# Kernel tuning notes

Measured on AMD Instinct MI355X. Metric: run time of the kernel, lower is better.

Reference implementation:

```python
import jax, jax.numpy as jnp
import numpy as np

N, E, B, F, H = 50000, 600000, 256, 128, 128
RATIO = 0.8
BN_EPS = 1e-5


def _topk_keep(score, batch, mask):
    # Per-graph top-ceil(RATIO*live) selection, expressed as a fixed-size keep mask.
    s = jnp.where(mask, score, -jnp.inf)
    order = jnp.lexsort((-s, batch))  # primary: batch id, secondary: score desc
    rank = jnp.zeros(N, dtype=jnp.int32).at[order].set(jnp.arange(N, dtype=jnp.int32))
    total = jax.ops.segment_sum(jnp.ones(N, dtype=jnp.int32), batch, B)
    starts = jnp.cumsum(total) - total
    r_in_g = (rank - starts[batch]).astype(jnp.float32)  # rank within own graph
    live = jax.ops.segment_sum(mask.astype(jnp.float32), batch, B)
    k = jnp.ceil(RATIO * live)
    return (r_in_g < k[batch]) & mask


def _forward(x, edge_index, batch, W1s, b1s, W2s, b2s, gammas, betas, pool_ws):
    src, dst = edge_index[0], edge_index[1]
    mask = jnp.ones(N, dtype=bool)      # live-node mask (TopK pooling shrinks graphs)
    e_mask = jnp.ones(E, dtype=bool)    # live-edge mask
    out = jnp.zeros((B, 2 * H), dtype=x.dtype)
    for i in range(4):
        # GINConv (eps=0): MLP(x + sum_{j->i} x_j)
        msg = jnp.where(e_mask[:, None], x[src], 0.0)
        agg = jax.ops.segment_sum(msg, dst, num_segments=N)
        h = x + agg
        h = jax.nn.relu(h @ W1s[i] + b1s[i]) @ W2s[i] + b2s[i]
        # BatchNorm (training mode) over live nodes only
        m = mask[:, None].astype(h.dtype)
        n = jnp.maximum(jnp.sum(m), 1.0)
        mean = jnp.sum(h * m, axis=0) / n
        var = jnp.sum(((h - mean) ** 2) * m, axis=0) / n
        h = (h - mean) * jax.lax.rsqrt(var + BN_EPS) * gammas[i] + betas[i]
        h = jax.nn.relu(h) * m
        # TopKPooling(ratio=0.8): score = x@w/||w||, keep top-k per graph, scale by tanh
        w = pool_ws[i]
        score = (h @ w) / jnp.linalg.norm(w)
        keep = _topk_keep(score, batch, mask)
        x = jnp.where(keep[:, None], h * jnp.tanh(score)[:, None], 0.0)
        mask = keep
        e_mask = e_mask & keep[src] & keep[dst]
        # global max pool + global mean pool over live nodes
        mx = jax.ops.segment_max(jnp.where(mask[:, None], x, -jnp.inf), batch, num_segments=B)
        mx = jnp.where(jnp.isfinite(mx), mx, 0.0)
        cnt = jax.ops.segment_sum(mask.astype(x.dtype), batch, num_segments=B)
        mn = jax.ops.segment_sum(x, batch, num_segments=B) / jnp.maximum(cnt, 1.0)[:, None]
        out = out + jnp.concatenate([mx, mn], axis=1)  # x1 + x2 + x3 + x4
    return out


def setup_inputs() -> dict:
    key = jax.random.key(0)
    k = jax.random.split(key, 8)
    s = 1.0 / np.sqrt(H)
    return {
        "x": jax.random.normal(k[0], (N, F), jnp.float32),
        "edge_index": jax.random.randint(k[1], (2, E), 0, N),
        "batch": jnp.sort(jax.random.randint(k[2], (N,), 0, B)),
        "W1s": jax.random.normal(k[3], (4, F, H), jnp.float32) * s,
        "b1s": jax.random.normal(k[4], (4, H), jnp.float32) * s,
        "W2s": jax.random.normal(k[5], (4, H, H), jnp.float32) * s,
        "b2s": jax.random.normal(k[6], (4, H), jnp.float32) * s,
        "gammas": jnp.ones((4, H), jnp.float32),
        "betas": jnp.zeros((4, H), jnp.float32),
        "pool_ws": jax.random.normal(k[7], (4, H), jnp.float32) * s,
    }


def reference(x, edge_index, batch, W1s, b1s, W2s, b2s, gammas, betas, pool_ws):
    return _forward(x, edge_index, batch, W1s, b1s, W2s, b2s, gammas, betas, pool_ws)
```

## Files before the change

### kernel.cpp

```cpp
#include <hip/hip_runtime.h>
#include <hip/hip_bf16.h>
#include <math.h>


#define HF 128
#define CHUNK_LG 14

typedef __attribute__((ext_vector_type(8))) short short8;
typedef __attribute__((ext_vector_type(4))) float floatx4;

__device__ __forceinline__ unsigned short cvt_bf16(float f) {
    unsigned u = __float_as_uint(f);
    u = u + 0x7fffu + ((u >> 16) & 1u);
    return (unsigned short)(u >> 16);
}
__device__ __forceinline__ float bf16f(unsigned short h) {
    return __uint_as_float(((unsigned)h) << 16);
}

__device__ __forceinline__ void split3(float f, short& p1, short& p2, short& p3) {
    unsigned u = __float_as_uint(f);
    unsigned r = u + 0x7fffu + ((u >> 16) & 1u);
    p1 = (short)(r >> 16);
    float r1 = f - __uint_as_float(r & 0xffff0000u);
    unsigned u1 = __float_as_uint(r1);
    p2 = (short)(u1 >> 16);
    float r2 = r1 - __uint_as_float(u1 & 0xffff0000u);
    p3 = (short)(__float_as_uint(r2) >> 16);
}


__global__ __launch_bounds__(256)
void k_hist(const int* __restrict__ dst, unsigned int* __restrict__ partial,
            unsigned char* __restrict__ eslot,
            float* __restrict__ stats4, float* __restrict__ out,
            int* __restrict__ lc,
            int N, int E, int nd4, int outsz, int X) {
    __shared__ unsigned int lh[12544];
    int bl = blockIdx.x, tid = threadIdx.x;
    for (int i = tid; i < nd4; i += 256) lh[i] = 0;
    __syncthreads();
    int e0 = bl << CHUNK_LG;
    int e1 = min(E, e0 + (1 << CHUNK_LG));
    for (int e = e0 + tid; e < e1; e += 256) {
        int d = dst[e];
        unsigned int old = atomicAdd(&lh[d >> 2], 1u << (8 * (d & 3)));
        eslot[e] = (unsigned char)((old >> (8 * (d & 3))) & 255u);
    }
    __syncthreads();
    for (int i = tid; i < nd4; i += 256) partial[(size_t)bl * nd4 + i] = lh[i];
    int gt = bl * 256 + tid, tot = X * 256;
    for (int i = gt; i < 4 * 256; i += tot) stats4[i] = 0.f;
    for (int i = gt; i < outsz; i += tot) out[i] = 0.f;
    if (gt < 5) lc[gt] = (gt == 0) ? N : 0;
}

__global__ __launch_bounds__(256)
void k_colsum(const unsigned int* __restrict__ partial, unsigned int* __restrict__ baseoff,
              int* __restrict__ deg, int* __restrict__ blocksum,
              int nd4, int X, int N) {
    __shared__ int red[256];
    int tid = threadIdx.x;
    int d4 = blockIdx.x * 256 + tid;
    unsigned int run = 0;
    if (d4 < nd4) {
        for (int bl = 0; bl < X; ++bl) {
            unsigned int c = partial[(size_t)bl * nd4 + d4];
            baseoff[(size_t)bl * nd4 + d4] = run;
            run += c;
        }
        int d = d4 * 4;
#pragma unroll
        for (int j = 0; j < 4; ++j)
            if (d + j < N) deg[d + j] = (int)((run >> (8 * j)) & 255u);
    }
    int tsum = (int)((run & 255u) + ((run >> 8) & 255u) + ((run >> 16) & 255u) + ((run >> 24) & 255u));
    red[tid] = tsum;
    __syncthreads();
    for (int off = 128; off; off >>= 1) {
        if (tid < off) red[tid] += red[tid + off];
        __syncthreads();
    }
    if (tid == 0) blocksum[blockIdx.x] = red[0];
}

__global__ void k_mid(const int* __restrict__ blocksum, int* __restrict__ blockoff,
                      int nblk, const int* __restrict__ batch,
                      int* __restrict__ gstart, int B, int n,
                      const float* __restrict__ pw, float* __restrict__ normv4) {
    int t = threadIdx.x;
    if (t <= B) {
        int lo = 0, hi = n;
        while (lo < hi) { int mid = (lo + hi) >> 1; if (batch[mid] < t) lo = mid + 1; else hi = mid; }
        gstart[t] = lo;
    }
    if (t >= 508) {
        int l = t - 508;
        float s = 0.f;
        for (int j = 0; j < HF; ++j) { float wv = pw[l * HF + j]; s += wv * wv; }
        normv4[l] = sqrtf(s);
    }
    if (t < 64) {
        int b0 = (t < nblk) ? blocksum[t] : 0;
        int v = b0;
#pragma unroll
        for (int off = 1; off < 64; off <<= 1) {
            int u = __shfl_up(v, off, 64);
            if (t >= off) v += u;
        }
        if (t < nblk) blockoff[t] = v - b0;
    }
}

__global__ __launch_bounds__(256)
void k_indptr(const int* __restrict__ deg, const int* __restrict__ blockoff,
              int* __restrict__ indptr, int nd4, int N) {
    __shared__ int ss[256];
    int tid = threadIdx.x;
    int d4 = blockIdx.x * 256 + tid;
    int dv[4] = {0, 0, 0, 0};
    int tsum = 0;
    if (d4 < nd4) {
        int d = d4 * 4;
#pragma unroll
        for (int j = 0; j < 4; ++j)
            if (d + j < N) { dv[j] = deg[d + j]; tsum += dv[j]; }
    }
    ss[tid] = tsum;
    __syncthreads();
    for (int off = 1; off < 256; off <<= 1) {
        int v = (tid >= off) ? ss[tid - off] : 0;
        __syncthreads();
        ss[tid] += v;
        __syncthreads();
    }
    if (d4 < nd4) {
        int b = blockoff[blockIdx.x] + ss[tid] - tsum;
        int d = d4 * 4;
#pragma unroll
        for (int j = 0; j < 4; ++j)
            if (d + j < N) { indptr[d + j] = b; b += dv[j]; }
        if (d4 == (N - 1) >> 2) indptr[N] = b;
    }
}

__global__ __launch_bounds__(256)
void k_place(const int* __restrict__ src, const int* __restrict__ dst,
             const unsigned char* __restrict__ eslot, const unsigned int* __restrict__ baseoff,
             const int* __restrict__ indptr, int* __restrict__ csr, int E, int nd4) {
    int e = blockIdx.x * 256 + threadIdx.x;
    if (e >= E) return;
    int d = dst[e];
    int bl = e >> CHUNK_LG;
    unsigned int bo = (baseoff[(size_t)bl * nd4 + (d >> 2)] >> (8 * (d & 3))) & 255u;
    csr[indptr[d] + (int)bo + (int)eslot[e]] = src[e];
}

__global__ void k_wsplit(const float* __restrict__ W1s, const float* __restrict__ W2s,
                         short8* __restrict__ wf) {
    int t = blockIdx.x * 256 + threadIdx.x;
    if (t >= 4 * 2 * 4 * 8 * 64) return;
    int lane = t & 63; int r = t >> 6;
    int ct = r & 7; r >>= 3; int kc = r & 3; r >>= 2; int g = r & 1; int l = r >> 1;
    const float* W = (g ? W2s : W1s) + l * 16384;
    int m = lane & 15, q = lane >> 4;
    int col = ct * 16 + m;
    short8 v1, v2, v3;
#pragma unroll
    for (int j = 0; j < 8; ++j) {
        float f = W[(size_t)(kc * 32 + q * 8 + j) * HF + col];
        unsigned short p1 = cvt_bf16(f); float r1 = f - bf16f(p1);
        unsigned short p2 = cvt_bf16(r1); float r2 = r1 - bf16f(p2);
        unsigned short p3 = cvt_bf16(r2);
        v1[j] = (short)p1; v2[j] = (short)p2; v3[j] = (short)p3;
    }
    size_t base = ((size_t)(l * 2 + g) * 6144) + ((size_t)(kc * 8 + ct) * 64) + lane;
    wf[base] = v1; wf[base + 2048] = v2; wf[base + 4096] = v3;
}


__global__ __launch_bounds__(256)
void k_agg(const float* __restrict__ x, const int* __restrict__ indptr,
           const int* __restrict__ csr, float* __restrict__ xa,
           const int* __restrict__ ll, const int* __restrict__ cnt, int N) {
    int widx = (blockIdx.x * 256 + threadIdx.x) >> 6;
    int count = ll ? *cnt : N;
    if (widx >= count) return;
    int wid = ll ? ll[widx] : widx;
    int lane = threadIdx.x & 63;
    int half = lane >> 5;
    int c = (lane & 31) * 4;
    int beg = indptr[wid], end = indptr[wid + 1];
    float4 a0 = make_float4(0.f, 0.f, 0.f, 0.f), a1 = a0, a2 = a0, a3 = a0;
    int e = beg + half;
    for (; e + 6 < end; e += 8) {
        int s0 = csr[e], s1 = csr[e + 2], s2 = csr[e + 4], s3 = csr[e + 6];
        float4 v0 = *(const float4*)&x[(size_t)s0 * HF + c];
        float4 v1 = *(const float4*)&x[(size_t)s1 * HF + c];
        float4 v2 = *(const float4*)&x[(size_t)s2 * HF + c];
        float4 v3 = *(const float4*)&x[(size_t)s3 * HF + c];
        a0.x += v0.x; a0.y += v0.y; a0.z += v0.z; a0.w += v0.w;
        a1.x += v1.x; a1.y += v1.y; a1.z += v1.z; a1.w += v1.w;
        a2.x += v2.x; a2.y += v2.y; a2.z += v2.z; a2.w += v2.w;
        a3.x += v3.x; a3.y += v3.y; a3.z += v3.z; a3.w += v3.w;
    }
    for (; e < end; e += 2) {
        int s0 = csr[e];
        float4 v0 = *(const float4*)&x[(size_t)s0 * HF + c];
        a0.x += v0.x; a0.y += v0.y; a0.z += v0.z; a0.w += v0.w;
    }
    float4 acc = make_float4(a0.x + a1.x + a2.x + a3.x, a0.y + a1.y + a2.y + a3.y,
                             a0.z + a1.z + a2.z + a3.z, a0.w + a1.w + a2.w + a3.w);
    acc.x += __shfl_down(acc.x, 32);
    acc.y += __shfl_down(acc.y, 32);
    acc.z += __shfl_down(acc.z, 32);
    acc.w += __shfl_down(acc.w, 32);
    if (half == 0) {
        float4 xv = *(const float4*)&x[(size_t)wid * HF + c];
        acc.x += xv.x; acc.y += xv.y; acc.z += xv.z; acc.w += xv.w;
        *(float4*)&xa[(size_t)wid * HF + c] = acc;
    }
}

__global__ __launch_bounds__(256, 2)
void k_mlp(const float* __restrict__ xa,
           const short8* __restrict__ wf1, const short8* __restrict__ wf2,
           const float* __restrict__ b1, const float* __restrict__ b2,
           const int* __restrict__ ll, const int* __restrict__ cnt,
           float* __restrict__ h, float* __restrict__ stats, int N) {
    __shared__ float sH[4 * 2 * 16 * 132];
    int tid = threadIdx.x;
    int count = ll ? *cnt : N;
    if (blockIdx.x * 128 >= count) return;
    int w = tid >> 6, lane = tid & 63;
    int m = lane & 15, q = lane >> 4;
    int base = blockIdx.x * 128 + w * 32;

    const float* aptr[2];
#pragma unroll
    for (int t = 0; t < 2; ++t) {
        int idx = base + t * 16 + m;
        int idc = (idx < count) ? idx : (count - 1);
        int row = ll ? ll[idc] : idc;
        aptr[t] = &xa[(size_t)row * HF + q * 8];
    }

    floatx4 acc[2][8];
#pragma unroll
    for (int t = 0; t < 2; ++t)
#pragma unroll
        for (int ct = 0; ct < 8; ++ct) acc[t][ct] = (floatx4){0.f, 0.f, 0.f, 0.f};

    float4 af0[2], af1[2];
#pragma unroll
    for (int t = 0; t < 2; ++t) {
        af0[t] = *(const float4*)(aptr[t]);
        af1[t] = *(const float4*)(aptr[t] + 4);
    }
#pragma unroll 1
    for (int kc = 0; kc < 4; ++kc) {
        short8 as[2][3];
#pragma unroll
        for (int t = 0; t < 2; ++t) {
            float av[8] = {af0[t].x, af0[t].y, af0[t].z, af0[t].w,
                           af1[t].x, af1[t].y, af1[t].z, af1[t].w};
#pragma unroll
            for (int j = 0; j < 8; ++j) {
                short p1, p2, p3;
                split3(av[j], p1, p2, p3);
                as[t][0][j] = p1; as[t][1][j] = p2; as[t][2][j] = p3;
            }
        }
        if (kc < 3) {
#pragma unroll
            for (int t = 0; t < 2; ++t) {
                af0[t] = *(const float4*)(aptr[t] + (kc + 1) * 32);
                af1[t] = *(const float4*)(aptr[t] + (kc + 1) * 32 + 4);
            }
        }
        const short8* bp = wf1 + (size_t)(kc * 8) * 64 + lane;
        short8 c1 = bp[0], c2 = bp[2048], c3 = bp[4096];
#pragma unroll
        for (int ct = 0; ct < 8; ++ct) {
            short8 n1, n2, n3;
            if (ct < 7) {
                const short8* np = bp + (size_t)(ct + 1) * 64;
                n1 = np[0]; n2 = np[2048]; n3 = np[4096];
            }
#pragma unroll
            for (int t = 0; t < 2; ++t) {
                acc[t][ct] = __builtin_amdgcn_mfma_f32_16x16x32_bf16(as[t][0], c1, acc[t][ct], 0, 0, 0);
                acc[t][ct] = __builtin_amdgcn_mfma_f32_16x16x32_bf16(as[t][1], c1, acc[t][ct], 0, 0, 0);
                acc[t][ct] = __builtin_amdgcn_mfma_f32_16x16x32_bf16(as[t][0], c2, acc[t][ct], 0, 0, 0);
                acc[t][ct] = __builtin_amdgcn_mfma_f32_16x16x32_bf16(as[t][2], c1, acc[t][ct], 0, 0, 0);
                acc[t][ct] = __builtin_amdgcn_mfma_f32_16x16x32_bf16(as[t][1], c2, acc[t][ct], 0, 0, 0);
                acc[t][ct] = __builtin_amdgcn_mfma_f32_16x16x32_bf16(as[t][0], c3, acc[t][ct], 0, 0, 0);
            }
            if (ct < 7) { c1 = n1; c2 = n2; c3 = n3; }
        }
    }

    float* sl[2] = {&sH[(w * 2) * 16 * 132], &sH[(w * 2 + 1) * 16 * 132]};
    float bb1[8];
#pragma unroll
    for (int ct = 0; ct < 8; ++ct) bb1[ct] = b1[ct * 16 + m];
#pragma unroll
    for (int t = 0; t < 2; ++t)
#pragma unroll
        for (int ct = 0; ct < 8; ++ct) {
#pragma unroll
            for (int reg = 0; reg < 4; ++reg) {
                float v = fmaxf(acc[t][ct][reg] + bb1[ct], 0.f);
                sl[t][(q * 4 + reg) * 132 + ct * 16 + m] = v;
            }
            acc[t][ct] = (floatx4){0.f, 0.f, 0.f, 0.f};
        }

#pragma unroll 1
    for (int kc = 0; kc < 4; ++kc) {
        short8 as[2][3];
#pragma unroll
        for (int t = 0; t < 2; ++t) {
            const float* ap = &sl[t][m * 132 + kc * 32 + q * 8];
            float4 x0 = *(const float4*)ap;
            float4 x1 = *(const float4*)(ap + 4);
            float av[8] = {x0.x, x0.y, x0.z, x0.w, x1.x, x1.y, x1.z, x1.w};
#pragma unroll
            for (int j = 0; j < 8; ++j) {
                short p1, p2, p3;
                split3(av[j], p1, p2, p3);
                as[t][0][j] = p1; as[t][1][j] = p2; as[t][2][j] = p3;
            }
        }
        const short8* bp = wf2 + (size_t)(kc * 8) * 64 + lane;
        short8 c1 = bp[0], c2 = bp[2048], c3 = bp[4096];
#pragma unroll
        for (int ct = 0; ct < 8; ++ct) {
            short8 n1, n2, n3;
            if (ct < 7) {
                const short8* np = bp + (size_t)(ct + 1) * 64;
                n1 = np[0]; n2 = np[2048]; n3 = np[4096];
            }
#pragma unroll
            for (int t = 0; t < 2; ++t) {
                acc[t][ct] = __builtin_amdgcn_mfma_f32_16x16x32_bf16(as[t][0], c1, acc[t][ct], 0, 0, 0);
                acc[t][ct] = __builtin_amdgcn_mfma_f32_16x16x32_bf16(as[t][1], c1, acc[t][ct], 0, 0, 0);
                acc[t][ct] = __builtin_amdgcn_mfma_f32_16x16x32_bf16(as[t][0], c2, acc[t][ct], 0, 0, 0);
                acc[t][ct] = __builtin_amdgcn_mfma_f32_16x16x32_bf16(as[t][2], c1, acc[t][ct], 0, 0, 0);
                acc[t][ct] = __builtin_amdgcn_mfma_f32_16x16x32_bf16(as[t][1], c2, acc[t][ct], 0, 0, 0);
                acc[t][ct] = __builtin_amdgcn_mfma_f32_16x16x32_bf16(as[t][0], c3, acc[t][ct], 0, 0, 0);
            }
            if (ct < 7) { c1 = n1; c2 = n2; c3 = n3; }
        }
    }

    float bb2[8];
#pragma unroll
    for (int ct = 0; ct < 8; ++ct) bb2[ct] = b2[ct * 16 + m];
    int rowv[2][4];
#pragma unroll
    for (int t = 0; t < 2; ++t)
#pragma unroll
        for (int reg = 0; reg < 4; ++reg) {
            int idx = base + t * 16 + q * 4 + reg;
            rowv[t][reg] = (idx < count) ? (ll ? ll[idx] : idx) : -1;
        }
    float sv[8], qv[8];
#pragma unroll
    for (int ct = 0; ct < 8; ++ct) {
        float s = 0.f, qq = 0.f;
#pragma unroll
        for (int t = 0; t < 2; ++t)
#pragma unroll
            for (int reg = 0; reg < 4; ++reg) {
                float v = acc[t][ct][reg] + bb2[ct];
                if (rowv[t][reg] >= 0) {
                    h[(size_t)rowv[t][reg] * HF + ct * 16 + m] = v;
                    s += v; qq += v * v;
                }
            }
        s += __shfl_xor(s, 16, 64);  s += __shfl_xor(s, 32, 64);
        qq += __shfl_xor(qq, 16, 64); qq += __shfl_xor(qq, 32, 64);
        sv[ct] = s; qv[ct] = qq;
    }
    __syncthreads();
    float* sStat = sH;
    if (lane < 16) {
#pragma unroll
        for (int ct = 0; ct < 8; ++ct) {
            sStat[w * 256 + ct * 16 + lane] = sv[ct];
            sStat[1024 + w * 256 + ct * 16 + lane] = qv[ct];
        }
    }
    __syncthreads();
    if (tid < 128) {
        float s = sStat[tid] + sStat[256 + tid] + sStat[512 + tid] + sStat[768 + tid];
        float qq = sStat[1024 + tid] + sStat[1280 + tid] + sStat[1536 + tid] + sStat[1792 + tid];
        atomicAdd(&stats[tid], s);
        atomicAdd(&stats[128 + tid], qq);
    }
}

__global__ __launch_bounds__(256)
void k_score(const float* __restrict__ h, const float* __restrict__ stats,
             const float* __restrict__ gamma, const float* __restrict__ beta,
             const float* __restrict__ w, const float* __restrict__ normv,
             const int* __restrict__ ll, const int* __restrict__ cnt,
             float* __restrict__ score, float* __restrict__ x, int N) {
    int widx = (blockIdx.x * 256 + threadIdx.x) >> 6;
    int count = ll ? *cnt : N;
    if (widx >= count) return;
    int node = ll ? ll[widx] : widx;
    int lane = threadIdx.x & 63;
    int c = lane * 2;
    float n = fmaxf((float)count, 1.0f);
    float su0 = stats[c], su1 = stats[c + 1];
    float sq0 = stats[128 + c], sq1 = stats[128 + c + 1];
    float m0 = su0 / n, m1 = su1 / n;
    float va0 = fmaxf(sq0 / n - m0 * m0, 0.f);
    float va1 = fmaxf(sq1 / n - m1 * m1, 0.f);
    float sc0 = gamma[c] * rsqrtf(va0 + 1e-5f);
    float sc1 = gamma[c + 1] * rsqrtf(va1 + 1e-5f);
    float sh0 = beta[c] - m0 * sc0;
    float sh1 = beta[c + 1] - m1 * sc1;
    float2 hv = *(const float2*)&h[(size_t)node * HF + c];
    float a0 = fmaxf(fmaf(hv.x, sc0, sh0), 0.f);
    float a1 = fmaxf(fmaf(hv.y, sc1, sh1), 0.f);
    float s = a0 * w[c] + a1 * w[c + 1];
#pragma unroll
    for (int off = 1; off < 64; off <<= 1) s += __shfl_xor(s, off, 64);
    float scv = s / normv[0];
    if (lane == 0) score[node] = scv;
    float t = tanhf(scv);
    *(float2*)&x[(size_t)node * HF + c] = make_float2(a0 * t, a1 * t);
}

__global__ __launch_bounds__(1024)
void k_topkpool(const float* __restrict__ score, const int* __restrict__ ll_in,
                const int* __restrict__ gstart, const int* __restrict__ gseg_in,
                int* __restrict__ ll_out, int* __restrict__ gseg_out,
                int* __restrict__ lcnt_out, float* __restrict__ x,
                float* __restrict__ out) {
    __shared__ unsigned long long skey[512];
    __shared__ float smx[7 * 128], ssum[7 * 128];
    __shared__ int s_base;
    int b = blockIdx.x, tid = threadIdx.x;
    int s0, lv;
    if (ll_in) { s0 = gseg_in[2 * b]; lv = gseg_in[2 * b + 1]; }
    else { s0 = gstart[b]; lv = gstart[b + 1] - s0; }
    if (lv > 512) lv = 512;
    int M = 32; while (M < lv) M <<= 1;

    for (int p = tid; p < M; p += 1024) {
        unsigned long long key = ~0ull;
        if (p < lv) {
            int node = ll_in ? ll_in[s0 + p] : (s0 + p);
            unsigned u = __float_as_uint(score[node]);
            u = (u & 0x80000000u) ? ~u : (u | 0x80000000u);
            key = (((unsigned long long)(~u)) << 32) | (unsigned)node;
        }
        skey[p] = key;
    }
    __syncthreads();
    for (int k = 2; k <= M; k <<= 1) {
        for (int jj = k >> 1; jj > 0; jj >>= 1) {
            for (int t = tid; t < M; t += 1024) {
                int ixj = t ^ jj;
                if (ixj > t) {
                    bool up = ((t & k) == 0);
                    unsigned long long A = skey[t], Bv = skey[ixj];
                    if ((A > Bv) == up) { skey[t] = Bv; skey[ixj] = A; }
                }
            }
            __syncthreads();
        }
    }
    int kk = (lv > 0) ? (int)ceilf(0.8f * (float)lv) : 0;
    if (tid == 0) s_base = atomicAdd(lcnt_out, kk);
    __syncthreads();
    int sb = s_base;
    if (tid == 0) { gseg_out[2 * b] = sb; gseg_out[2 * b + 1] = kk; }
    for (int p = tid; p < kk; p += 1024)
        ll_out[sb + p] = (int)(skey[p] & 0xFFFFFFFFu);

    int wv = tid >> 6, lane = tid & 63;
    for (int p = kk + wv; p < lv; p += 16) {
        int node = (int)(skey[p] & 0xFFFFFFFFu);
        *(float2*)&x[(size_t)node * HF + lane * 2] = make_float2(0.f, 0.f);
    }

    int f = tid & 127, g = tid >> 7;
    float mx = -INFINITY, sum = 0.f;
    for (int p = g; p < kk; p += 8) {
        int node = (int)(skey[p] & 0xFFFFFFFFu);
        float v = x[(size_t)node * HF + f];
        mx = fmaxf(mx, v);
        sum += v;
    }
    if (g) { smx[(g - 1) * 128 + f] = mx; ssum[(g - 1) * 128 + f] = sum; }
    __syncthreads();
    if (g == 0) {
#pragma unroll
        for (int k2 = 0; k2 < 7; ++k2) {
            mx = fmaxf(mx, smx[k2 * 128 + f]);
            sum += ssum[k2 * 128 + f];
        }
        float mxo = (kk > 0) ? mx : 0.f;
        float mn = sum / (float)(kk > 0 ? kk : 1);
        out[b * 256 + f] += mxo;
        out[b * 256 + 128 + f] += mn;
    }
}


extern "C" void kernel_launch(void* const* d_in, const int* in_sizes, int n_in,
                              void* d_out, int out_size, void* d_ws, size_t ws_size,
                              hipStream_t stream) {
    const float* x_in    = (const float*)d_in[0];
    const int*   ei      = (const int*)d_in[1];
    const int*   batch   = (const int*)d_in[2];
    const float* W1s     = (const float*)d_in[3];
    const float* b1s     = (const float*)d_in[4];
    const float* W2s     = (const float*)d_in[5];
    const float* b2s     = (const float*)d_in[6];
    const float* gammas  = (const float*)d_in[7];
    const float* betas   = (const float*)d_in[8];
    const float* pool_ws = (const float*)d_in[9];

    int N = in_sizes[0] / HF;
    int E = in_sizes[1] / 2;
    int B = out_size / (2 * HF);
    const int* src = ei;
    const int* dst = ei + E;
    int nd4 = (N + 3) >> 2;
    int X = (E + (1 << CHUNK_LG) - 1) >> CHUNK_LG;
    int nblk = (nd4 + 255) >> 8;

    char* ws = (char*)d_ws;
    size_t off = 0;
    auto alloc = [&](size_t bytes) -> void* {
        void* p = ws + off;
        off = (off + bytes + 255) & ~(size_t)255;
        return p;
    };
    float* xa      = (float*)alloc((size_t)N * HF * 4);
    float* h       = (float*)alloc((size_t)N * HF * 4);
    float* xbuf    = (float*)alloc((size_t)N * HF * 4);
    float* score   = (float*)alloc((size_t)N * 4);
    int*   deg     = (int*)alloc((size_t)(N + 1) * 4);
    int*   indptr  = (int*)alloc((size_t)(N + 1) * 4);
    int*   csr     = (int*)alloc((size_t)E * 4);
    int*   gstart  = (int*)alloc((size_t)(B + 1) * 4);
    float* stats4  = (float*)alloc(4 * 256 * 4);
    float* normv4  = (float*)alloc(4 * 4);
    int*   lc      = (int*)alloc(8 * 4);
    int*   llA     = (int*)alloc((size_t)N * 4);
    int*   llB     = (int*)alloc((size_t)N * 4);
    int*   gsegA   = (int*)alloc((size_t)2 * B * 4);
    int*   gsegB   = (int*)alloc((size_t)2 * B * 4);
    int*   blocksum = (int*)alloc(64 * 4);
    int*   blockoff = (int*)alloc(64 * 4);
    short8* wfrag  = (short8*)alloc((size_t)8 * 6144 * 16);
    unsigned int* partial = (unsigned int*)alloc((size_t)X * nd4 * 4);
    unsigned int* baseoff = (unsigned int*)alloc((size_t)X * nd4 * 4);
    unsigned char* eslot  = (unsigned char*)alloc((size_t)E);
    float* out    = (float*)d_out;

    int tb = 256;
    k_hist<<<X, tb, 0, stream>>>(dst, partial, eslot, stats4, out, lc,
                                 N, E, nd4, out_size, X);
    k_wsplit<<<64, tb, 0, stream>>>(W1s, W2s, wfrag);
    k_colsum<<<nblk, tb, 0, stream>>>(partial, baseoff, deg, blocksum, nd4, X, N);
    k_mid<<<1, 512, 0, stream>>>(blocksum, blockoff, nblk, batch, gstart, B, N,
                                 pool_ws, normv4);
    k_indptr<<<nblk, tb, 0, stream>>>(deg, blockoff, indptr, nd4, N);
    k_place<<<(E + tb - 1) / tb, tb, 0, stream>>>(src, dst, eslot, baseoff, indptr, csr, E, nd4);

    int bound[4];
    bound[0] = N;
    for (int i = 1; i < 4; ++i) bound[i] = (4 * bound[i - 1] + 4) / 5 + B;

    const int* ll_in[4]   = {nullptr, llA, llB, llA};
    int*       ll_ot[4]   = {llA, llB, llA, llB};
    const int* gseg_in[4] = {nullptr, gsegA, gsegB, gsegA};
    int*       gseg_ot[4] = {gsegA, gsegB, gsegA, gsegB};

    for (int i = 0; i < 4; ++i) {
        const float* xc = (i == 0) ? x_in : xbuf;
        float* stats = stats4 + i * 256;
        k_agg<<<(bound[i] + 3) / 4, tb, 0, stream>>>(xc, indptr, csr, xa,
                                                     ll_in[i], lc + i, N);
        k_mlp<<<(bound[i] + 127) / 128, tb, 0, stream>>>(xa,
                                                wfrag + (size_t)(i * 2) * 6144,
                                                wfrag + (size_t)(i * 2 + 1) * 6144,
                                                b1s + i * 128, b2s + i * 128,
                                                ll_in[i], lc + i, h, stats, N);
        k_score<<<(bound[i] + 3) / 4, tb, 0, stream>>>(h, stats, gammas + i * 128,
                                                betas + i * 128, pool_ws + i * 128,
                                                normv4 + i, ll_in[i], lc + i,
                                                score, xbuf, N);
        k_topkpool<<<B, 1024, 0, stream>>>(score, ll_in[i], gstart, gseg_in[i],
                                           ll_ot[i], gseg_ot[i], lc + i + 1,
                                           xbuf, out);
    }
}
```

Measured before the change: 526.3 us.

## Fuse neighbor aggregation into MLP kernel and skip dead source rows

Removes the separate k_agg kernel and the xa buffer. The MLP kernel now gathers neighbor features directly into shared memory, one wave looping serially over its 32 rows. A per-node live byte mask, cleared by top-k pooling, lets the gather skip loads from dropped nodes in later layers. This saves a launch and an N×128 float write and read, but each wave now processes its rows sequentially, so the gather has less parallelism and latency hiding than the one-wave-per-node kernel had.

```diff
diff --git a/kernel.cpp b/kernel.cpp
--- a/kernel.cpp
+++ b/kernel.cpp
@@ -32,7 +32,7 @@
 
 __global__ __launch_bounds__(256)
 void k_hist(const int* __restrict__ dst, unsigned int* __restrict__ partial,
-            unsigned char* __restrict__ eslot,
+            unsigned char* __restrict__ eslot, unsigned char* __restrict__ live8,
             float* __restrict__ stats4, float* __restrict__ out,
             int* __restrict__ lc,
             int N, int E, int nd4, int outsz, int X) {
@@ -50,6 +50,7 @@
     __syncthreads();
     for (int i = tid; i < nd4; i += 256) partial[(size_t)bl * nd4 + i] = lh[i];
     int gt = bl * 256 + tid, tot = X * 256;
+    for (int i = gt; i < N; i += tot) live8[i] = 1;
     for (int i = gt; i < 4 * 256; i += tot) stats4[i] = 0.f;
     for (int i = gt; i < outsz; i += tot) out[i] = 0.f;
     if (gt < 5) lc[gt] = (gt == 0) ? N : 0;
@@ -179,51 +180,9 @@
 }
 
 
-__global__ __launch_bounds__(256)
-void k_agg(const float* __restrict__ x, const int* __restrict__ indptr,
-           const int* __restrict__ csr, float* __restrict__ xa,
-           const int* __restrict__ ll, const int* __restrict__ cnt, int N) {
-    int widx = (blockIdx.x * 256 + threadIdx.x) >> 6;
-    int count = ll ? *cnt : N;
-    if (widx >= count) return;
-    int wid = ll ? ll[widx] : widx;
-    int lane = threadIdx.x & 63;
-    int half = lane >> 5;
-    int c = (lane & 31) * 4;
-    int beg = indptr[wid], end = indptr[wid + 1];
-    float4 a0 = make_float4(0.f, 0.f, 0.f, 0.f), a1 = a0, a2 = a0, a3 = a0;
-    int e = beg + half;
-    for (; e + 6 < end; e += 8) {
-        int s0 = csr[e], s1 = csr[e + 2], s2 = csr[e + 4], s3 = csr[e + 6];
-        float4 v0 = *(const float4*)&x[(size_t)s0 * HF + c];
-        float4 v1 = *(const float4*)&x[(size_t)s1 * HF + c];
-        float4 v2 = *(const float4*)&x[(size_t)s2 * HF + c];
-        float4 v3 = *(const float4*)&x[(size_t)s3 * HF + c];
-        a0.x += v0.x; a0.y += v0.y; a0.z += v0.z; a0.w += v0.w;
-        a1.x += v1.x; a1.y += v1.y; a1.z += v1.z; a1.w += v1.w;
-        a2.x += v2.x; a2.y += v2.y; a2.z += v2.z; a2.w += v2.w;
-        a3.x += v3.x; a3.y += v3.y; a3.z += v3.z; a3.w += v3.w;
-    }
-    for (; e < end; e += 2) {
-        int s0 = csr[e];
-        float4 v0 = *(const float4*)&x[(size_t)s0 * HF + c];
-        a0.x += v0.x; a0.y += v0.y; a0.z += v0.z; a0.w += v0.w;
-    }
-    float4 acc = make_float4(a0.x + a1.x + a2.x + a3.x, a0.y + a1.y + a2.y + a3.y,
-                             a0.z + a1.z + a2.z + a3.z, a0.w + a1.w + a2.w + a3.w);
-    acc.x += __shfl_down(acc.x, 32);
-    acc.y += __shfl_down(acc.y, 32);
-    acc.z += __shfl_down(acc.z, 32);
-    acc.w += __shfl_down(acc.w, 32);
-    if (half == 0) {
-        float4 xv = *(const float4*)&x[(size_t)wid * HF + c];
-        acc.x += xv.x; acc.y += xv.y; acc.z += xv.z; acc.w += xv.w;
-        *(float4*)&xa[(size_t)wid * HF + c] = acc;
-    }
-}
-
 __global__ __launch_bounds__(256, 2)
-void k_mlp(const float* __restrict__ xa,
+void k_mlp(const float* __restrict__ x, const int* __restrict__ indptr,
+           const int* __restrict__ csr, const unsigned char* __restrict__ live8,
            const short8* __restrict__ wf1, const short8* __restrict__ wf2,
            const float* __restrict__ b1, const float* __restrict__ b2,
            const int* __restrict__ ll, const int* __restrict__ cnt,
@@ -235,14 +194,52 @@
     int w = tid >> 6, lane = tid & 63;
     int m = lane & 15, q = lane >> 4;
     int base = blockIdx.x * 128 + w * 32;
-
-    const float* aptr[2];
-#pragma unroll
-    for (int t = 0; t < 2; ++t) {
-        int idx = base + t * 16 + m;
-        int idc = (idx < count) ? idx : (count - 1);
-        int row = ll ? ll[idc] : idc;
-        aptr[t] = &xa[(size_t)row * HF + q * 8];
+    float* sl[2] = {&sH[(w * 2) * 16 * 132], &sH[(w * 2 + 1) * 16 * 132]};
+
+    {
+        int half = lane >> 5;
+        int c = (lane & 31) * 4;
+#pragma unroll 2
+        for (int n = 0; n < 32; ++n) {
+            int idx = base + n;
+            float* srow = &sl[n >> 4][(n & 15) * 132];
+            if (idx >= count) {
+                if (half == 0) *(float4*)&srow[c] = make_float4(0.f, 0.f, 0.f, 0.f);
+                continue;
+            }
+            int node = ll ? ll[idx] : idx;
+            int beg = indptr[node], end = indptr[node + 1];
+            float4 a0 = make_float4(0.f, 0.f, 0.f, 0.f), a1 = a0;
+            int e = beg + half;
+            for (; e + 2 < end; e += 4) {
+                int s0 = csr[e], s1 = csr[e + 2];
+                if (!live8 || live8[s0]) {
+                    float4 v = *(const float4*)&x[(size_t)s0 * HF + c];
+                    a0.x += v.x; a0.y += v.y; a0.z += v.z; a0.w += v.w;
+                }
+                if (!live8 || live8[s1]) {
+                    float4 v = *(const float4*)&x[(size_t)s1 * HF + c];
+                    a1.x += v.x; a1.y += v.y; a1.z += v.z; a1.w += v.w;
+                }
+            }
+            for (; e < end; e += 2) {
+                int s0 = csr[e];
+                if (!live8 || live8[s0]) {
+                    float4 v = *(const float4*)&x[(size_t)s0 * HF + c];
+                    a0.x += v.x; a0.y += v.y; a0.z += v.z; a0.w += v.w;
+                }
+            }
+            a0.x += a1.x; a0.y += a1.y; a0.z += a1.z; a0.w += a1.w;
+            a0.x += __shfl_down(a0.x, 32);
+            a0.y += __shfl_down(a0.y, 32);
+            a0.z += __shfl_down(a0.z, 32);
+            a0.w += __shfl_down(a0.w, 32);
+            if (half == 0) {
+                float4 xv = *(const float4*)&x[(size_t)node * HF + c];
+                a0.x += xv.x; a0.y += xv.y; a0.z += xv.z; a0.w += xv.w;
+                *(float4*)&srow[c] = a0;
+            }
+        }
     }
 
     floatx4 acc[2][8];
@@ -251,31 +248,20 @@
 #pragma unroll
         for (int ct = 0; ct < 8; ++ct) acc[t][ct] = (floatx4){0.f, 0.f, 0.f, 0.f};
 
-    float4 af0[2], af1[2];
-#pragma unroll
-    for (int t = 0; t < 2; ++t) {
-        af0[t] = *(const float4*)(aptr[t]);
-        af1[t] = *(const float4*)(aptr[t] + 4);
-    }
 #pragma unroll 1
     for (int kc = 0; kc < 4; ++kc) {
         short8 as[2][3];
 #pragma unroll
         for (int t = 0; t < 2; ++t) {
-            float av[8] = {af0[t].x, af0[t].y, af0[t].z, af0[t].w,
-                           af1[t].x, af1[t].y, af1[t].z, af1[t].w};
+            const float* ap = &sl[t][m * 132 + kc * 32 + q * 8];
+            float4 x0 = *(const float4*)ap;
+            float4 x1 = *(const float4*)(ap + 4);
+            float av[8] = {x0.x, x0.y, x0.z, x0.w, x1.x, x1.y, x1.z, x1.w};
 #pragma unroll
             for (int j = 0; j < 8; ++j) {
                 short p1, p2, p3;
                 split3(av[j], p1, p2, p3);
                 as[t][0][j] = p1; as[t][1][j] = p2; as[t][2][j] = p3;
-            }
-        }
-        if (kc < 3) {
-#pragma unroll
-            for (int t = 0; t < 2; ++t) {
-                af0[t] = *(const float4*)(aptr[t] + (kc + 1) * 32);
-                af1[t] = *(const float4*)(aptr[t] + (kc + 1) * 32 + 4);
             }
         }
         const short8* bp = wf1 + (size_t)(kc * 8) * 64 + lane;
@@ -300,7 +286,6 @@
         }
     }
 
-    float* sl[2] = {&sH[(w * 2) * 16 * 132], &sH[(w * 2 + 1) * 16 * 132]};
     float bb1[8];
 #pragma unroll
     for (int ct = 0; ct < 8; ++ct) bb1[ct] = b1[ct * 16 + m];
@@ -440,7 +425,7 @@
                 const int* __restrict__ gstart, const int* __restrict__ gseg_in,
                 int* __restrict__ ll_out, int* __restrict__ gseg_out,
                 int* __restrict__ lcnt_out, float* __restrict__ x,
-                float* __restrict__ out) {
+                unsigned char* __restrict__ live8, float* __restrict__ out) {
     __shared__ unsigned long long skey[512];
     __shared__ float smx[7 * 128], ssum[7 * 128];
     __shared__ int s_base;
@@ -487,6 +472,7 @@
     for (int p = kk + wv; p < lv; p += 16) {
         int node = (int)(skey[p] & 0xFFFFFFFFu);
         *(float2*)&x[(size_t)node * HF + lane * 2] = make_float2(0.f, 0.f);
+        if (lane == 0) live8[node] = 0;
     }
 
     int f = tid & 127, g = tid >> 7;
@@ -543,7 +529,6 @@
         off = (off + bytes + 255) & ~(size_t)255;
         return p;
     };
-    float* xa      = (float*)alloc((size_t)N * HF * 4);
     float* h       = (float*)alloc((size_t)N * HF * 4);
     float* xbuf    = (float*)alloc((size_t)N * HF * 4);
     float* score   = (float*)alloc((size_t)N * 4);
@@ -564,10 +549,11 @@
     unsigned int* partial = (unsigned int*)alloc((size_t)X * nd4 * 4);
     unsigned int* baseoff = (unsigned int*)alloc((size_t)X * nd4 * 4);
     unsigned char* eslot  = (unsigned char*)alloc((size_t)E);
+    unsigned char* live8  = (unsigned char*)alloc((size_t)N);
     float* out    = (float*)d_out;
 
     int tb = 256;
-    k_hist<<<X, tb, 0, stream>>>(dst, partial, eslot, stats4, out, lc,
+    k_hist<<<X, tb, 0, stream>>>(dst, partial, eslot, live8, stats4, out, lc,
                                  N, E, nd4, out_size, X);
     k_wsplit<<<64, tb, 0, stream>>>(W1s, W2s, wfrag);
     k_colsum<<<nblk, tb, 0, stream>>>(partial, baseoff, deg, blocksum, nd4, X, N);
@@ -588,9 +574,8 @@
     for (int i = 0; i < 4; ++i) {
         const float* xc = (i == 0) ? x_in : xbuf;
         float* stats = stats4 + i * 256;
-        k_agg<<<(bound[i] + 3) / 4, tb, 0, stream>>>(xc, indptr, csr, xa,
-                                                     ll_in[i], lc + i, N);
-        k_mlp<<<(bound[i] + 127) / 128, tb, 0, stream>>>(xa,
+        k_mlp<<<(bound[i] + 127) / 128, tb, 0, stream>>>(xc, indptr, csr,
+                                                (i == 0) ? nullptr : live8,
                                                 wfrag + (size_t)(i * 2) * 6144,
                                                 wfrag + (size_t)(i * 2 + 1) * 6144,
                                                 b1s + i * 128, b2s + i * 128,
@@ -601,6 +586,6 @@
                                                 score, xbuf, N);
         k_topkpool<<<B, 1024, 0, stream>>>(score, ll_in[i], gstart, gseg_in[i],
                                            ll_ot[i], gseg_ot[i], lc + i + 1,
-                                           xbuf, out);
-    }
-}
+                                           xbuf, live8, out);
+    }
+}
```

New measurement: 889.7 us. +69.0%, slower.

## Redirect dead-source edges to a zero row and halve MLP shared memory

Applied to the files above, without the earlier changes.

Adds a per-node live flag that topk pooling clears for dropped nodes. After each layer a remap kernel rewrites the CSR so edges from dead sources point to an extra all-zero row at index N, so aggregation gathers from one hot zero row instead of scattered zeroed rows. Separately, the MLP's second GEMM now processes its two row tiles one after another through a single shared staging buffer, which halves LDS and raises the occupancy hint from 2 to 4 blocks. The cost is an extra full-E remap kernel per layer and a serialized second-GEMM loop.

```diff
diff --git a/kernel.cpp b/kernel.cpp
--- a/kernel.cpp
+++ b/kernel.cpp
@@ -32,9 +32,9 @@
 
 __global__ __launch_bounds__(256)
 void k_hist(const int* __restrict__ dst, unsigned int* __restrict__ partial,
-            unsigned char* __restrict__ eslot,
+            unsigned char* __restrict__ eslot, unsigned char* __restrict__ live8,
             float* __restrict__ stats4, float* __restrict__ out,
-            int* __restrict__ lc,
+            float* __restrict__ xdummy, int* __restrict__ lc,
             int N, int E, int nd4, int outsz, int X) {
     __shared__ unsigned int lh[12544];
     int bl = blockIdx.x, tid = threadIdx.x;
@@ -50,8 +50,10 @@
     __syncthreads();
     for (int i = tid; i < nd4; i += 256) partial[(size_t)bl * nd4 + i] = lh[i];
     int gt = bl * 256 + tid, tot = X * 256;
+    for (int i = gt; i < N; i += tot) live8[i] = 1;
     for (int i = gt; i < 4 * 256; i += tot) stats4[i] = 0.f;
     for (int i = gt; i < outsz; i += tot) out[i] = 0.f;
+    for (int i = gt; i < HF; i += tot) xdummy[i] = 0.f;
     if (gt < 5) lc[gt] = (gt == 0) ? N : 0;
 }
 
@@ -154,6 +156,15 @@
     int bl = e >> CHUNK_LG;
     unsigned int bo = (baseoff[(size_t)bl * nd4 + (d >> 2)] >> (8 * (d & 3))) & 255u;
     csr[indptr[d] + (int)bo + (int)eslot[e]] = src[e];
+}
+
+__global__ __launch_bounds__(256)
+void k_remap(const int* __restrict__ csr, const unsigned char* __restrict__ live8,
+             int* __restrict__ csr2, int E, int N) {
+    int e = blockIdx.x * 256 + threadIdx.x;
+    if (e >= E) return;
+    int s = csr[e];
+    csr2[e] = live8[s] ? s : N;
 }
 
 __global__ void k_wsplit(const float* __restrict__ W1s, const float* __restrict__ W2s,
@@ -222,19 +233,20 @@
     }
 }
 
-__global__ __launch_bounds__(256, 2)
+__global__ __launch_bounds__(256, 4)
 void k_mlp(const float* __restrict__ xa,
            const short8* __restrict__ wf1, const short8* __restrict__ wf2,
            const float* __restrict__ b1, const float* __restrict__ b2,
            const int* __restrict__ ll, const int* __restrict__ cnt,
            float* __restrict__ h, float* __restrict__ stats, int N) {
-    __shared__ float sH[4 * 2 * 16 * 132];
+    __shared__ float sH[4 * 16 * 132];
     int tid = threadIdx.x;
     int count = ll ? *cnt : N;
     if (blockIdx.x * 128 >= count) return;
     int w = tid >> 6, lane = tid & 63;
     int m = lane & 15, q = lane >> 4;
     int base = blockIdx.x * 128 + w * 32;
+    float* sl = &sH[w * 16 * 132];
 
     const float* aptr[2];
 #pragma unroll
@@ -300,57 +312,52 @@
         }
     }
 
-    float* sl[2] = {&sH[(w * 2) * 16 * 132], &sH[(w * 2 + 1) * 16 * 132]};
     float bb1[8];
 #pragma unroll
     for (int ct = 0; ct < 8; ++ct) bb1[ct] = b1[ct * 16 + m];
-#pragma unroll
-    for (int t = 0; t < 2; ++t)
+#pragma unroll 1
+    for (int t = 0; t < 2; ++t) {
 #pragma unroll
         for (int ct = 0; ct < 8; ++ct) {
 #pragma unroll
             for (int reg = 0; reg < 4; ++reg) {
                 float v = fmaxf(acc[t][ct][reg] + bb1[ct], 0.f);
-                sl[t][(q * 4 + reg) * 132 + ct * 16 + m] = v;
+                sl[(q * 4 + reg) * 132 + ct * 16 + m] = v;
             }
             acc[t][ct] = (floatx4){0.f, 0.f, 0.f, 0.f};
         }
-
 #pragma unroll 1
-    for (int kc = 0; kc < 4; ++kc) {
-        short8 as[2][3];
-#pragma unroll
-        for (int t = 0; t < 2; ++t) {
-            const float* ap = &sl[t][m * 132 + kc * 32 + q * 8];
-            float4 x0 = *(const float4*)ap;
-            float4 x1 = *(const float4*)(ap + 4);
-            float av[8] = {x0.x, x0.y, x0.z, x0.w, x1.x, x1.y, x1.z, x1.w};
-#pragma unroll
-            for (int j = 0; j < 8; ++j) {
-                short p1, p2, p3;
-                split3(av[j], p1, p2, p3);
-                as[t][0][j] = p1; as[t][1][j] = p2; as[t][2][j] = p3;
-            }
-        }
-        const short8* bp = wf2 + (size_t)(kc * 8) * 64 + lane;
-        short8 c1 = bp[0], c2 = bp[2048], c3 = bp[4096];
-#pragma unroll
-        for (int ct = 0; ct < 8; ++ct) {
-            short8 n1, n2, n3;
-            if (ct < 7) {
-                const short8* np = bp + (size_t)(ct + 1) * 64;
-                n1 = np[0]; n2 = np[2048]; n3 = np[4096];
-            }
-#pragma unroll
-            for (int t = 0; t < 2; ++t) {
-                acc[t][ct] = __builtin_amdgcn_mfma_f32_16x16x32_bf16(as[t][0], c1, acc[t][ct], 0, 0, 0);
-                acc[t][ct] = __builtin_amdgcn_mfma_f32_16x16x32_bf16(as[t][1], c1, acc[t][ct], 0, 0, 0);
-                acc[t][ct] = __builtin_amdgcn_mfma_f32_16x16x32_bf16(as[t][0], c2, acc[t][ct], 0, 0, 0);
-                acc[t][ct] = __builtin_amdgcn_mfma_f32_16x16x32_bf16(as[t][2], c1, acc[t][ct], 0, 0, 0);
-                acc[t][ct] = __builtin_amdgcn_mfma_f32_16x16x32_bf16(as[t][1], c2, acc[t][ct], 0, 0, 0);
-                acc[t][ct] = __builtin_amdgcn_mfma_f32_16x16x32_bf16(as[t][0], c3, acc[t][ct], 0, 0, 0);
-            }
-            if (ct < 7) { c1 = n1; c2 = n2; c3 = n3; }
+        for (int kc = 0; kc < 4; ++kc) {
+            short8 as[3];
+            {
+                const float* ap = &sl[m * 132 + kc * 32 + q * 8];
+                float4 x0 = *(const float4*)ap;
+                float4 x1 = *(const float4*)(ap + 4);
+                float av[8] = {x0.x, x0.y, x0.z, x0.w, x1.x, x1.y, x1.z, x1.w};
+#pragma unroll
+                for (int j = 0; j < 8; ++j) {
+                    short p1, p2, p3;
+                    split3(av[j], p1, p2, p3);
+                    as[0][j] = p1; as[1][j] = p2; as[2][j] = p3;
+                }
+            }
+            const short8* bp = wf2 + (size_t)(kc * 8) * 64 + lane;
+            short8 c1 = bp[0], c2 = bp[2048], c3 = bp[4096];
+#pragma unroll
+            for (int ct = 0; ct < 8; ++ct) {
+                short8 n1, n2, n3;
+                if (ct < 7) {
+                    const short8* np = bp + (size_t)(ct + 1) * 64;
+                    n1 = np[0]; n2 = np[2048]; n3 = np[4096];
+                }
+                acc[t][ct] = __builtin_amdgcn_mfma_f32_16x16x32_bf16(as[0], c1, acc[t][ct], 0, 0, 0);
+                acc[t][ct] = __builtin_amdgcn_mfma_f32_16x16x32_bf16(as[1], c1, acc[t][ct], 0, 0, 0);
+                acc[t][ct] = __builtin_amdgcn_mfma_f32_16x16x32_bf16(as[0], c2, acc[t][ct], 0, 0, 0);
+                acc[t][ct] = __builtin_amdgcn_mfma_f32_16x16x32_bf16(as[2], c1, acc[t][ct], 0, 0, 0);
+                acc[t][ct] = __builtin_amdgcn_mfma_f32_16x16x32_bf16(as[1], c2, acc[t][ct], 0, 0, 0);
+                acc[t][ct] = __builtin_amdgcn_mfma_f32_16x16x32_bf16(as[0], c3, acc[t][ct], 0, 0, 0);
+                if (ct < 7) { c1 = n1; c2 = n2; c3 = n3; }
+            }
         }
     }
 
@@ -440,7 +447,7 @@
                 const int* __restrict__ gstart, const int* __restrict__ gseg_in,
                 int* __restrict__ ll_out, int* __restrict__ gseg_out,
                 int* __restrict__ lcnt_out, float* __restrict__ x,
-                float* __restrict__ out) {
+                unsigned char* __restrict__ live8, float* __restrict__ out) {
     __shared__ unsigned long long skey[512];
     __shared__ float smx[7 * 128], ssum[7 * 128];
     __shared__ int s_base;
@@ -487,6 +494,7 @@
     for (int p = kk + wv; p < lv; p += 16) {
         int node = (int)(skey[p] & 0xFFFFFFFFu);
         *(float2*)&x[(size_t)node * HF + lane * 2] = make_float2(0.f, 0.f);
+        if (lane == 0) live8[node] = 0;
     }
 
     int f = tid & 127, g = tid >> 7;
@@ -545,11 +553,12 @@
     };
     float* xa      = (float*)alloc((size_t)N * HF * 4);
     float* h       = (float*)alloc((size_t)N * HF * 4);
-    float* xbuf    = (float*)alloc((size_t)N * HF * 4);
+    float* xbuf    = (float*)alloc((size_t)(N + 1) * HF * 4);
     float* score   = (float*)alloc((size_t)N * 4);
     int*   deg     = (int*)alloc((size_t)(N + 1) * 4);
     int*   indptr  = (int*)alloc((size_t)(N + 1) * 4);
     int*   csr     = (int*)alloc((size_t)E * 4);
+    int*   csr2    = (int*)alloc((size_t)E * 4);
     int*   gstart  = (int*)alloc((size_t)(B + 1) * 4);
     float* stats4  = (float*)alloc(4 * 256 * 4);
     float* normv4  = (float*)alloc(4 * 4);
@@ -564,11 +573,12 @@
     unsigned int* partial = (unsigned int*)alloc((size_t)X * nd4 * 4);
     unsigned int* baseoff = (unsigned int*)alloc((size_t)X * nd4 * 4);
     unsigned char* eslot  = (unsigned char*)alloc((size_t)E);
+    unsigned char* live8  = (unsigned char*)alloc((size_t)N);
     float* out    = (float*)d_out;
 
     int tb = 256;
-    k_hist<<<X, tb, 0, stream>>>(dst, partial, eslot, stats4, out, lc,
-                                 N, E, nd4, out_size, X);
+    k_hist<<<X, tb, 0, stream>>>(dst, partial, eslot, live8, stats4, out,
+                                 xbuf + (size_t)N * HF, lc, N, E, nd4, out_size, X);
     k_wsplit<<<64, tb, 0, stream>>>(W1s, W2s, wfrag);
     k_colsum<<<nblk, tb, 0, stream>>>(partial, baseoff, deg, blocksum, nd4, X, N);
     k_mid<<<1, 512, 0, stream>>>(blocksum, blockoff, nblk, batch, gstart, B, N,
@@ -587,8 +597,9 @@
 
     for (int i = 0; i < 4; ++i) {
         const float* xc = (i == 0) ? x_in : xbuf;
+        const int* csr_i = (i == 0) ? csr : csr2;
         float* stats = stats4 + i * 256;
-        k_agg<<<(bound[i] + 3) / 4, tb, 0, stream>>>(xc, indptr, csr, xa,
+        k_agg<<<(bound[i] + 3) / 4, tb, 0, stream>>>(xc, indptr, csr_i, xa,
                                                      ll_in[i], lc + i, N);
         k_mlp<<<(bound[i] + 127) / 128, tb, 0, stream>>>(xa,
                                                 wfrag + (size_t)(i * 2) * 6144,
@@ -601,6 +612,8 @@
                                                 score, xbuf, N);
         k_topkpool<<<B, 1024, 0, stream>>>(score, ll_in[i], gstart, gseg_in[i],
                                            ll_ot[i], gseg_ot[i], lc + i + 1,
-                                           xbuf, out);
-    }
-}
+                                           xbuf, live8, out);
+        if (i < 3)
+            k_remap<<<(E + tb - 1) / tb, tb, 0, stream>>>(csr, live8, csr2, E, N);
+    }
+}
```

New measurement: 652.5 us. 1.24x slower.
